# Kernel tuning notes

Measured on AMD Instinct MI355X. Metric: run time of the kernel, lower is better.

The kernel has to match this reference:

```python
import jax, jax.numpy as jnp
import numpy as np

N_LAYERS, HEADS, D_IN, D_OUT, T, D, DFF = 4, 8, 16, 3, 1024, 512, 2048
D_HEAD = D // HEADS


def sinusoidal_pos_enc(t, d):
    # Faithful to the source: base = pos / 10000**(emb_idx/d); sin on even cols, cos on odd cols
    pos = jnp.arange(t, dtype=jnp.float32)[:, None]
    emb = jnp.arange(d, dtype=jnp.float32)[None, :]
    base = pos / jnp.power(10000.0, emb / d)
    even = (jnp.arange(d) % 2 == 0)[None, :]
    return jnp.where(even, jnp.sin(base), jnp.cos(base))  # (t, d)


def layer_norm(x, g, b, eps=1e-5):
    m = x.mean(-1, keepdims=True)
    v = ((x - m) ** 2).mean(-1, keepdims=True)
    return (x - m) / jnp.sqrt(v + eps) * g + b


def setup_inputs() -> dict:
    key = jax.random.key(0)
    ks = iter(jax.random.split(key, 24))
    s = 0.02
    inp = {}
    inp['x'] = jax.random.normal(next(ks), (16, T, D_IN), dtype=jnp.float32)
    inp['pad_mask'] = jax.random.randint(next(ks), (16, T), 0, 2, dtype=jnp.int32)
    inp['enc_W'] = jax.random.normal(next(ks), (D_IN, D), dtype=jnp.float32) * s
    inp['enc_b'] = jnp.zeros((D,), jnp.float32)
    for name in ['Wq', 'Wk', 'Wv', 'Wo']:
        inp[name] = jax.random.normal(next(ks), (N_LAYERS, D, D), dtype=jnp.float32) * s
    inp['ff_W1'] = jax.random.normal(next(ks), (N_LAYERS, D, DFF), dtype=jnp.float32) * s
    inp['ff_b1'] = jnp.zeros((N_LAYERS, DFF), jnp.float32)
    inp['ff_W2'] = jax.random.normal(next(ks), (N_LAYERS, DFF, D), dtype=jnp.float32) * s
    inp['ff_b2'] = jnp.zeros((N_LAYERS, D), jnp.float32)
    inp['ln1_g'] = jnp.ones((N_LAYERS, D), jnp.float32)
    inp['ln1_b'] = jnp.zeros((N_LAYERS, D), jnp.float32)
    inp['ln2_g'] = jnp.ones((N_LAYERS, D), jnp.float32)
    inp['ln2_b'] = jnp.zeros((N_LAYERS, D), jnp.float32)
    inp['out_W'] = jax.random.normal(next(ks), (D * T, D_OUT), dtype=jnp.float32) * s
    inp['out_b'] = jnp.zeros((D_OUT,), jnp.float32)
    return inp


def reference(x, enc_W, enc_b, Wq, Wk, Wv, Wo, ff_W1, ff_b1, ff_W2, ff_b2,
              ln1_g, ln1_b, ln2_g, ln2_b, out_W, out_b, pad_mask):
    n, t = x.shape[0], x.shape[1]
    # InputEncoding (linear) scaled by sqrt(d_model)
    h = (x @ enc_W + enc_b) * jnp.sqrt(jnp.float32(D))
    # Sinusoidal positional encoding, zeroed at masked (pad_mask==0) timesteps
    pe = sinusoidal_pos_enc(t, D)[None]  # (1, t, d)
    pe = jnp.where(pad_mask[..., None] == 0, 0.0, pe)  # (n, t, d)
    h = h + pe
    mask4 = (pad_mask[..., None, None] == 0)  # (n, t, 1, 1)
    for i in range(N_LAYERS):
        # --- MultiHeadAttention (faithful to source's transpose quirk) ---
        Qh = (h @ Wq[i]).reshape(n, t, HEADS, D_HEAD).swapaxes(2, 3)  # (n,t,dh,H)
        Kh = (h @ Wk[i]).reshape(n, t, HEADS, D_HEAD)                 # (n,t,H,dh)
        Vh = (h @ Wv[i]).reshape(n, t, HEADS, D_HEAD).swapaxes(2, 3)  # (n,t,dh,H)
        # energy: per-timestep (dh x dh), scaled by d_head**1/2 == d_head/2 (source precedence)
        energy = jnp.matmul(Qh, Kh) / (D_HEAD / 2.0)                  # (n,t,dh,dh)
        energy = jnp.where(mask4, -1e20, energy)
        attn = jax.nn.softmax(energy, axis=-1)
        head = jnp.matmul(attn, Vh)                                   # (n,t,dh,H)
        out = head.reshape(n, t, D) @ Wo[i]
        # residual + layer norm
        h = layer_norm(out + h, ln1_g[i], ln1_b[i])
        # --- FFN (relu) ---
        ff = jax.nn.relu(h @ ff_W1[i] + ff_b1[i]) @ ff_W2[i] + ff_b2[i]
        h = layer_norm(ff + h, ln2_g[i], ln2_b[i])
    # mode='train': flatten and project
    return h.reshape(n, -1) @ out_W + out_b  # (n, d_output)
```

## Files before the change

kernel.cpp:

```cpp
#include <hip/hip_runtime.h>
#include <cmath>

#define NB 16
#define TSEQ 1024
#define DIN 16
#define DM 512
#define DFFN 2048
#define NLAYERS 4
#define DOUTN 3
#define ROWS (NB*TSEQ)

typedef unsigned short u16;
typedef unsigned int   u32;
typedef short bf16x8 __attribute__((ext_vector_type(8)));
typedef u16   u16x4  __attribute__((ext_vector_type(4)));
typedef float f32x4  __attribute__((ext_vector_type(4)));

__device__ __forceinline__ float b2f(u16 v) { return __uint_as_float((unsigned)v << 16); }
__device__ __forceinline__ u16 f2b(float f) {
    unsigned u = __float_as_uint(f);
    return (u16)((u + 0x7FFFu + ((u >> 16) & 1u)) >> 16);
}

#define GLL(gp, lp) __builtin_amdgcn_global_load_lds( \
    (const __attribute__((address_space(1))) unsigned int*)(gp), \
    (__attribute__((address_space(3))) unsigned int*)(lp), 16, 0, 0)

template<int PERM>
__global__ __launch_bounds__(256) void transpose_cast(
    const float* __restrict__ in, u16* __restrict__ out,
    int K, int N, size_t in_lstride, size_t out_lstride)
{
    in  += (size_t)blockIdx.z * in_lstride;
    out += (size_t)blockIdx.z * out_lstride;
    __shared__ float t[32][33];
    int bk = blockIdx.x * 32, bn = blockIdx.y * 32;
    int x = threadIdx.x & 31, y = threadIdx.x >> 5;
    #pragma unroll
    for (int i = 0; i < 32; i += 8)
        t[y + i][x] = in[(size_t)(bk + y + i) * N + bn + x];
    __syncthreads();
    #pragma unroll
    for (int i = 0; i < 32; i += 8) {
        int row = bn + y + i;
        if (PERM) row = ((row & 63) << 3) | ((row >> 6) & 7);
        out[(size_t)row * K + bk + x] = f2b(t[x][y + i]);
    }
}

__global__ __launch_bounds__(128) void encode_kernel(
    const float* __restrict__ x, const int* __restrict__ pad,
    const float* __restrict__ W, const float* __restrict__ b,
    u16* __restrict__ h)
{
    int row = blockIdx.x;
    int t   = row & (TSEQ - 1);
    int c   = threadIdx.x * 4;
    float acc[4];
    #pragma unroll
    for (int j = 0; j < 4; ++j) acc[j] = b[c + j];
    const float* xr = x + (size_t)row * DIN;
    #pragma unroll
    for (int k = 0; k < DIN; ++k) {
        float xv = xr[k];
        const float* wr = W + (size_t)k * DM + c;
        #pragma unroll
        for (int j = 0; j < 4; ++j) acc[j] += xv * wr[j];
    }
    const float s = 22.62741699796952f;
    bool has_pe = (pad[row] != 0);
    u16x4 o;
    #pragma unroll
    for (int j = 0; j < 4; ++j) {
        acc[j] *= s;
        if (has_pe) {
            int d = c + j;
            float base = (float)t * powf(10000.0f, -(float)d * (1.0f/512.0f));
            acc[j] += ((d & 1) == 0) ? sinf(base) : cosf(base);
        }
        o[j] = f2b(acc[j]);
    }
    *(u16x4*)&h[(size_t)row * DM + c] = o;
}

template<int BIAS, int RELU>
__global__ __launch_bounds__(512, 4) void gemm_bf16(
    const u16* __restrict__ A, const u16* __restrict__ Bt,
    const float* __restrict__ bias, u16* __restrict__ C,
    int M, int N, int K)
{
    __shared__ u16 S[4][8192];
    const int tid  = threadIdx.x;
    const int lane = tid & 63;
    const int wid  = tid >> 6;
    const int wr   = wid >> 2;
    const int wc   = wid & 3;

    const int NY  = N >> 7;
    const int nwg = gridDim.x;
    const int cpx = nwg >> 3;
    const int bid = blockIdx.x;
    const int swz = (bid & 7) * cpx + (bid >> 3);
    const int bm  = (swz / NY) * 128;
    const int bn  = (swz % NY) * 128;

    const int srow8 = lane >> 3;
    const int sslot = lane & 7;
    const int scol  = ((sslot ^ srow8) * 8);
    const u16* Ag = A  + (size_t)(bm + wid * 16 + srow8) * K + scol;
    const u16* Bg = Bt + (size_t)(bn + wid * 16 + srow8) * K + scol;

    f32x4 acc[4][2];
    #pragma unroll
    for (int m = 0; m < 4; ++m)
        #pragma unroll
        for (int n = 0; n < 2; ++n)
            acc[m][n] = (f32x4){0.f, 0.f, 0.f, 0.f};

    const int fr  = lane & 15;
    const int grp = lane >> 4;

    auto STAGE = [&](int k0, int d) {
        u16* Al = S[d * 2 + 0] + wid * 1024;
        u16* Bl = S[d * 2 + 1] + wid * 1024;
        #pragma unroll
        for (int i = 0; i < 2; ++i) {
            GLL(Ag + (size_t)(i * 8) * K + k0, Al + i * 512);
            GLL(Bg + (size_t)(i * 8) * K + k0, Bl + i * 512);
        }
    };

    STAGE(0, 0);
    __syncthreads();

    int cur = 0;
    for (int k0 = 0; k0 < K; k0 += 64) {
        if (k0 + 64 < K) STAGE(k0 + 64, cur ^ 1);
        const u16* As = S[cur * 2 + 0];
        const u16* Bs = S[cur * 2 + 1];
        bf16x8 a[4][2];
        #pragma unroll
        for (int m = 0; m < 4; ++m) {
            int row = wr * 64 + m * 16 + fr;
            #pragma unroll
            for (int ks = 0; ks < 2; ++ks) {
                int slot = (ks * 4 + grp) ^ (row & 7);
                a[m][ks] = *(const bf16x8*)(As + row * 64 + slot * 8);
            }
        }
        #pragma unroll
        for (int n = 0; n < 2; ++n) {
            bf16x8 b[2];
            int row = wc * 32 + n * 16 + fr;
            #pragma unroll
            for (int ks = 0; ks < 2; ++ks) {
                int slot = (ks * 4 + grp) ^ (row & 7);
                b[ks] = *(const bf16x8*)(Bs + row * 64 + slot * 8);
            }
            #pragma unroll
            for (int m = 0; m < 4; ++m) {
                acc[m][n] = __builtin_amdgcn_mfma_f32_16x16x32_bf16(a[m][0], b[0], acc[m][n], 0, 0, 0);
                acc[m][n] = __builtin_amdgcn_mfma_f32_16x16x32_bf16(a[m][1], b[1], acc[m][n], 0, 0, 0);
            }
        }
        __syncthreads();
        cur ^= 1;
    }

    float bb[2] = {0.f, 0.f};
    if (BIAS) {
        #pragma unroll
        for (int n = 0; n < 2; ++n) bb[n] = bias[bn + wc * 32 + n * 16 + fr];
    }
    #pragma unroll
    for (int m = 0; m < 4; ++m) {
        #pragma unroll
        for (int n = 0; n < 2; ++n) {
            int col = bn + wc * 32 + n * 16 + fr;
            #pragma unroll
            for (int j = 0; j < 4; ++j) {
                int row = bm + wr * 64 + m * 16 + grp * 4 + j;
                float v = acc[m][n][j];
                if (BIAS) v += bb[n];
                if (RELU) v = fmaxf(v, 0.f);
                C[(size_t)row * N + col] = f2b(v);
            }
        }
    }
}

__global__ __launch_bounds__(256) void attn_mfma(
    const u16* __restrict__ QKV, const int* __restrict__ pad,
    u16* __restrict__ O)
{
    constexpr int WLDS = 2560;
    __shared__ u16 sh[4 * WLDS];
    const int wid  = threadIdx.x >> 6;
    const int lane = threadIdx.x & 63;
    const int site = blockIdx.x * 4 + wid;
    u16* P2 = sh + wid * WLDS;
    u16* Ol = P2 + 2048;

    const u16* base = QKV + (size_t)site * 1536;
    const int fr  = lane & 15;
    const int grp = lane >> 4;
    const bf16x8 zb = {0,0,0,0,0,0,0,0};
    const f32x4  zf = {0.f,0.f,0.f,0.f};

    if (pad[site] == 0) {
        bf16x8 vv = *(const bf16x8*)(base + 1024 + lane * 8);
        float s = 0.f;
        #pragma unroll
        for (int j = 0; j < 8; ++j) s += b2f((u16)vv[j]);
        s += __shfl_xor(s, 1); s += __shfl_xor(s, 2); s += __shfl_xor(s, 4);
        s *= (1.0f / 64.0f);
        bf16x8 ov;
        #pragma unroll
        for (int h2 = 0; h2 < 8; ++h2) ov[h2] = (short)f2b(__shfl(s, h2 * 8));
        *(bf16x8*)(O + (size_t)site * DM + lane * 8) = ov;
        return;
    }

    bf16x8 kt[4];
    #pragma unroll
    for (int n = 0; n < 4; ++n)
        kt[n] = (grp == 0) ? *(const bf16x8*)(base + 512 + (n * 16 + fr) * 8) : zb;
    bf16x8 bv[2];
    #pragma unroll
    for (int ks = 0; ks < 2; ++ks)
        bv[ks] = (fr < 8) ? *(const bf16x8*)(base + 1024 + fr * 64 + ks * 32 + grp * 8) : zb;

    const int swz = (fr & 3) ^ (fr >> 2);
    u16x4 pk23[4][2];

    #pragma unroll
    for (int m = 0; m < 4; ++m) {
        bf16x8 aq = (grp == 0) ? *(const bf16x8*)(base + (m * 16 + fr) * 8) : zb;
        f32x4 ev[4];
        #pragma unroll
        for (int n = 0; n < 4; ++n)
            ev[n] = __builtin_amdgcn_mfma_f32_16x16x32_bf16(kt[n], aq, zf, 0, 0, 0);
        f32x4 t0, t1;
        #pragma unroll
        for (int j = 0; j < 4; ++j) { t0[j] = fmaxf(ev[0][j], ev[1][j]); t1[j] = fmaxf(ev[2][j], ev[3][j]); }
        float mx = -1e30f;
        #pragma unroll
        for (int j = 0; j < 4; ++j) mx = fmaxf(mx, fmaxf(t0[j], t1[j]));
        mx = fmaxf(mx, __shfl_xor(mx, 16));
        mx = fmaxf(mx, __shfl_xor(mx, 32));
        float p[4][4];
        float s = 0.f;
        #pragma unroll
        for (int n = 0; n < 4; ++n)
            #pragma unroll
            for (int j = 0; j < 4; ++j) {
                p[n][j] = __expf((ev[n][j] - mx) * 0.03125f);
                s += p[n][j];
            }
        s += __shfl_xor(s, 16);
        s += __shfl_xor(s, 32);
        float inv = 1.0f / s;
        u16x4 pk[4];
        #pragma unroll
        for (int n = 0; n < 4; ++n)
            #pragma unroll
            for (int j = 0; j < 4; ++j) pk[n][j] = f2b(p[n][j] * inv);
        int row = m * 16 + fr;
        #pragma unroll
        for (int n = 0; n < 2; ++n) {
            int chunk = (n * 2 + (grp >> 1)) ^ swz;
            *(u16x4*)(P2 + row * 32 + chunk * 8 + (grp & 1) * 4) = pk[n];
        }
        pk23[m][0] = pk[2];
        pk23[m][1] = pk[3];
    }

    f32x4 pv[4];
    #pragma unroll
    for (int m = 0; m < 4; ++m) {
        int row = m * 16 + fr;
        bf16x8 ap = *(const bf16x8*)(P2 + row * 32 + ((grp ^ swz) * 8));
        pv[m] = __builtin_amdgcn_mfma_f32_16x16x32_bf16(ap, bv[0], zf, 0, 0, 0);
    }
    asm volatile("s_waitcnt lgkmcnt(0)" ::: "memory");
    __builtin_amdgcn_sched_barrier(0);

    #pragma unroll
    for (int m = 0; m < 4; ++m) {
        int row = m * 16 + fr;
        #pragma unroll
        for (int n = 0; n < 2; ++n) {
            int chunk = (n * 2 + (grp >> 1)) ^ swz;
            *(u16x4*)(P2 + row * 32 + chunk * 8 + (grp & 1) * 4) = pk23[m][n];
        }
    }
    #pragma unroll
    for (int m = 0; m < 4; ++m) {
        int row = m * 16 + fr;
        bf16x8 ap = *(const bf16x8*)(P2 + row * 32 + ((grp ^ swz) * 8));
        pv[m] = __builtin_amdgcn_mfma_f32_16x16x32_bf16(ap, bv[1], pv[m], 0, 0, 0);
    }

    #pragma unroll
    for (int m = 0; m < 4; ++m)
        #pragma unroll
        for (int j = 0; j < 4; ++j) {
            int row = m * 16 + grp * 4 + j;
            if (fr < 8) Ol[row * 8 + fr] = f2b(pv[m][j]);
        }
    __syncthreads();
    bf16x8 o = *(const bf16x8*)(Ol + lane * 8);
    *(bf16x8*)(O + (size_t)site * DM + lane * 8) = o;
}

__global__ __launch_bounds__(256) void add_ln_kernel(
    const u16* __restrict__ A, u16* __restrict__ H,
    const float* __restrict__ g, const float* __restrict__ b)
{
    int row  = blockIdx.x * 4 + (threadIdx.x >> 6);
    int lane = threadIdx.x & 63;
    const u16* a = A + (size_t)row * DM + lane * 8;
    u16* h = H + (size_t)row * DM + lane * 8;
    bf16x8 av = *(const bf16x8*)a;
    bf16x8 hv = *(const bf16x8*)h;
    float v[8];
    float s = 0.f;
    #pragma unroll
    for (int j = 0; j < 8; ++j) { v[j] = b2f((u16)av[j]) + b2f((u16)hv[j]); s += v[j]; }
    #pragma unroll
    for (int off = 32; off > 0; off >>= 1) s += __shfl_xor(s, off, 64);
    float mean = s * (1.0f / 512.0f);
    float var = 0.f;
    #pragma unroll
    for (int j = 0; j < 8; ++j) { float d = v[j] - mean; var += d * d; }
    #pragma unroll
    for (int off = 32; off > 0; off >>= 1) var += __shfl_xor(var, off, 64);
    float rstd = rsqrtf(var * (1.0f / 512.0f) + 1e-5f);
    bf16x8 ov;
    #pragma unroll
    for (int j = 0; j < 8; ++j) {
        int d = lane * 8 + j;
        ov[j] = (short)f2b((v[j] - mean) * rstd * g[d] + b[d]);
    }
    *(bf16x8*)h = ov;
}

__global__ __launch_bounds__(256) void out_stage1(
    const u16* __restrict__ h, const float* __restrict__ W,
    float* __restrict__ partial)
{
    int b = blockIdx.x, s = blockIdx.y;
    int tid = threadIdx.x;
    const u16* hb = h + (size_t)b * (TSEQ * DM) + (size_t)s * 8192;
    const float* Wb = W + (size_t)s * 8192 * 3;
    float a0 = 0.f, a1 = 0.f, a2 = 0.f;
    #pragma unroll 4
    for (int it = 0; it < 32; ++it) {
        int i = it * 256 + tid;
        float hv = b2f(hb[i]);
        a0 += hv * Wb[i * 3 + 0];
        a1 += hv * Wb[i * 3 + 1];
        a2 += hv * Wb[i * 3 + 2];
    }
    __shared__ float red[3][256];
    red[0][tid] = a0; red[1][tid] = a1; red[2][tid] = a2;
    __syncthreads();
    for (int off = 128; off > 0; off >>= 1) {
        if (tid < off) {
            red[0][tid] += red[0][tid + off];
            red[1][tid] += red[1][tid + off];
            red[2][tid] += red[2][tid + off];
        }
        __syncthreads();
    }
    if (tid == 0) {
        partial[(b * 64 + s) * 3 + 0] = red[0][0];
        partial[(b * 64 + s) * 3 + 1] = red[1][0];
        partial[(b * 64 + s) * 3 + 2] = red[2][0];
    }
}

__global__ __launch_bounds__(64) void out_stage2(
    const float* __restrict__ partial, const float* __restrict__ ob,
    float* __restrict__ out)
{
    int t = threadIdx.x;
    if (t < NB * DOUTN) {
        int b = t / 3, o = t % 3;
        float s = ob[o];
        for (int k = 0; k < 64; ++k) s += partial[(b * 64 + k) * 3 + o];
        out[t] = s;
    }
}

extern "C" void kernel_launch(void* const* d_in, const int* in_sizes, int n_in,
                              void* d_out, int out_size, void* d_ws, size_t ws_size,
                              hipStream_t stream)
{
    const float* x    = (const float*)d_in[0];
    const int*   pad  = (const int*)  d_in[1];
    const float* encW = (const float*)d_in[2];
    const float* encB = (const float*)d_in[3];
    const float* Wq   = (const float*)d_in[4];
    const float* Wk   = (const float*)d_in[5];
    const float* Wv   = (const float*)d_in[6];
    const float* Wo   = (const float*)d_in[7];
    const float* fW1  = (const float*)d_in[8];
    const float* fb1  = (const float*)d_in[9];
    const float* fW2  = (const float*)d_in[10];
    const float* fb2  = (const float*)d_in[11];
    const float* l1g  = (const float*)d_in[12];
    const float* l1b  = (const float*)d_in[13];
    const float* l2g  = (const float*)d_in[14];
    const float* l2b  = (const float*)d_in[15];
    const float* outW = (const float*)d_in[16];
    const float* outB = (const float*)d_in[17];
    float* out = (float*)d_out;

    const size_t WL  = 3145728;
    const size_t BUF = (size_t)ROWS * DM;
    const size_t need = (4 * WL + 6 * BUF) * sizeof(u16);
    if (ws_size < need) return;
    u16* wt = (u16*)d_ws;
    u16* h  = wt + 4 * WL;
    u16* b0 = h  + BUF;
    u16* b3 = b0 + 3 * BUF;
    u16* b4 = b3 + BUF;

    transpose_cast<1><<<dim3(16,16,4), 256, 0, stream>>>(Wq,  wt + 0,       512,  512,  (size_t)512*512,  WL);
    transpose_cast<1><<<dim3(16,16,4), 256, 0, stream>>>(Wk,  wt + 262144,  512,  512,  (size_t)512*512,  WL);
    transpose_cast<0><<<dim3(16,16,4), 256, 0, stream>>>(Wv,  wt + 524288,  512,  512,  (size_t)512*512,  WL);
    transpose_cast<0><<<dim3(16,16,4), 256, 0, stream>>>(Wo,  wt + 786432,  512,  512,  (size_t)512*512,  WL);
    transpose_cast<0><<<dim3(16,64,4), 256, 0, stream>>>(fW1, wt + 1048576, 512,  2048, (size_t)512*2048, WL);
    transpose_cast<0><<<dim3(64,16,4), 256, 0, stream>>>(fW2, wt + 2097152, 2048, 512,  (size_t)2048*512, WL);

    encode_kernel<<<ROWS, 128, 0, stream>>>(x, pad, encW, encB, h);

    for (int l = 0; l < NLAYERS; ++l) {
        u16* wl = wt + (size_t)l * WL;
        gemm_bf16<0,0><<<dim3((ROWS/128)*(1536/128)), 512, 0, stream>>>(h, wl, nullptr, b0, ROWS, 1536, DM);
        attn_mfma<<<ROWS/4, 256, 0, stream>>>(b0, pad, b3);
        gemm_bf16<0,0><<<dim3((ROWS/128)*(DM/128)), 512, 0, stream>>>(b3, wl + 786432, nullptr, b4, ROWS, DM, DM);
        add_ln_kernel<<<ROWS/4, 256, 0, stream>>>(b4, h, l1g + l*DM, l1b + l*DM);
        gemm_bf16<1,1><<<dim3((ROWS/128)*(DFFN/128)), 512, 0, stream>>>(h, wl + 1048576, fb1 + (size_t)l*DFFN, b0, ROWS, DFFN, DM);
        gemm_bf16<1,0><<<dim3((ROWS/128)*(DM/128)), 512, 0, stream>>>(b0, wl + 2097152, fb2 + (size_t)l*DM, b4, ROWS, DM, DFFN);
        add_ln_kernel<<<ROWS/4, 256, 0, stream>>>(b4, h, l2g + l*DM, l2b + l*DM);
    }

    out_stage1<<<dim3(NB, 64), 256, 0, stream>>>(h, outW, (float*)b0);
    out_stage2<<<1, 64, 0, stream>>>((float*)b0, outB, out);
}
```

Baseline: 738.6 us.

## Add triple-buffered BK=32 GEMM with vmcnt-based waits for FFN matmuls

Adds a new GEMM kernel that stages 128x32 tiles of A and B into three LDS buffers with global_load_lds. It uses s_waitcnt vmcnt plus a single barrier per k-step, so loads for step t+2 overlap compute on step t. The smaller LDS footprint allows a launch bound of 6 waves per SIMD. The two FFN GEMMs use the new kernel, while the QKV and output projections keep the original 128x64 double-buffered kernel. The risk is more barriers per unit of K, and correctness of the tail handling depends on nt being of the form 3k+1 (K=512 gives 16, K=2048 gives 64, both fit).

```diff
diff --git a/kernel.cpp b/kernel.cpp
--- a/kernel.cpp
+++ b/kernel.cpp
@@ -26,6 +26,11 @@
     (const __attribute__((address_space(1))) unsigned int*)(gp), \
     (__attribute__((address_space(3))) unsigned int*)(lp), 16, 0, 0)
 
+#define WAITVM2() asm volatile("s_waitcnt vmcnt(2)" ::: "memory")
+#define WAITVM0() asm volatile("s_waitcnt vmcnt(0)" ::: "memory")
+#define BARR() do { asm volatile("" ::: "memory"); __builtin_amdgcn_s_barrier(); \
+                    asm volatile("" ::: "memory"); } while (0)
+
 template<int PERM>
 __global__ __launch_bounds__(256) void transpose_cast(
     const float* __restrict__ in, u16* __restrict__ out,
@@ -84,7 +89,7 @@
 }
 
 template<int BIAS, int RELU>
-__global__ __launch_bounds__(512, 4) void gemm_bf16(
+__global__ __launch_bounds__(512, 4) void gemm128(
     const u16* __restrict__ A, const u16* __restrict__ Bt,
     const float* __restrict__ bias, u16* __restrict__ C,
     int M, int N, int K)
@@ -166,6 +171,109 @@
         __syncthreads();
         cur ^= 1;
     }
+
+    float bb[2] = {0.f, 0.f};
+    if (BIAS) {
+        #pragma unroll
+        for (int n = 0; n < 2; ++n) bb[n] = bias[bn + wc * 32 + n * 16 + fr];
+    }
+    #pragma unroll
+    for (int m = 0; m < 4; ++m) {
+        #pragma unroll
+        for (int n = 0; n < 2; ++n) {
+            int col = bn + wc * 32 + n * 16 + fr;
+            #pragma unroll
+            for (int j = 0; j < 4; ++j) {
+                int row = bm + wr * 64 + m * 16 + grp * 4 + j;
+                float v = acc[m][n][j];
+                if (BIAS) v += bb[n];
+                if (RELU) v = fmaxf(v, 0.f);
+                C[(size_t)row * N + col] = f2b(v);
+            }
+        }
+    }
+}
+
+template<int BIAS, int RELU>
+__global__ __launch_bounds__(512, 6) void gemm3d(
+    const u16* __restrict__ A, const u16* __restrict__ Bt,
+    const float* __restrict__ bias, u16* __restrict__ C,
+    int M, int N, int K)
+{
+    __shared__ u16 S0a[4096], S0b[4096];
+    __shared__ u16 S1a[4096], S1b[4096];
+    __shared__ u16 S2a[4096], S2b[4096];
+    const int tid  = threadIdx.x;
+    const int lane = tid & 63;
+    const int wid  = tid >> 6;
+    const int wr   = wid >> 2;
+    const int wc   = wid & 3;
+
+    const int NY  = N >> 7;
+    const int nwg = gridDim.x;
+    const int cpx = nwg >> 3;
+    const int bid = blockIdx.x;
+    const int swz = (bid & 7) * cpx + (bid >> 3);
+    const int bm  = (swz / NY) * 128;
+    const int bn  = (swz % NY) * 128;
+
+    const int srow   = tid >> 2;
+    const int schunk = (tid & 3) ^ ((srow >> 1) & 3);
+    const u16* Ag = A  + (size_t)(bm + srow) * K + schunk * 8;
+    const u16* Bg = Bt + (size_t)(bn + srow) * K + schunk * 8;
+
+    f32x4 acc[4][2];
+    #pragma unroll
+    for (int m = 0; m < 4; ++m)
+        #pragma unroll
+        for (int n = 0; n < 2; ++n)
+            acc[m][n] = (f32x4){0.f, 0.f, 0.f, 0.f};
+
+    const int fr  = lane & 15;
+    const int grp = lane >> 4;
+
+    const int nt = K >> 5;
+
+#define STAGE3(kt, DA, DB) do { \
+        GLL(Ag + (size_t)(kt) * 32, DA + tid * 8); \
+        GLL(Bg + (size_t)(kt) * 32, DB + tid * 8); } while (0)
+
+#define STEP3(t, RA, RB, SA_, SB_, doStage, last) do { \
+        if (last) { WAITVM0(); } else { WAITVM2(); } \
+        BARR(); \
+        if (doStage) STAGE3((t) + 2, SA_, SB_); \
+        bf16x8 a_[4], b_[2]; \
+        _Pragma("unroll") \
+        for (int m = 0; m < 4; ++m) { \
+            int row = wr * 64 + m * 16 + fr; \
+            int slot = grp ^ ((row >> 1) & 3); \
+            a_[m] = *(const bf16x8*)(RA + row * 32 + slot * 8); \
+        } \
+        _Pragma("unroll") \
+        for (int n = 0; n < 2; ++n) { \
+            int row = wc * 32 + n * 16 + fr; \
+            int slot = grp ^ ((row >> 1) & 3); \
+            b_[n] = *(const bf16x8*)(RB + row * 32 + slot * 8); \
+        } \
+        _Pragma("unroll") \
+        for (int n = 0; n < 2; ++n) \
+            _Pragma("unroll") \
+            for (int m = 0; m < 4; ++m) \
+                acc[m][n] = __builtin_amdgcn_mfma_f32_16x16x32_bf16(a_[m], b_[n], acc[m][n], 0, 0, 0); \
+    } while (0)
+
+    STAGE3(0, S0a, S0b);
+    STAGE3(1, S1a, S1b);
+
+    for (int it = 0; it + 3 < nt; it += 3) {
+        STEP3(it + 0, S0a, S0b, S2a, S2b, (it + 2 < nt), false);
+        STEP3(it + 1, S1a, S1b, S0a, S0b, (it + 3 < nt), false);
+        STEP3(it + 2, S2a, S2b, S1a, S1b, (it + 4 < nt), false);
+    }
+    STEP3(nt - 1, S0a, S0b, S1a, S1b, false, true);
+
+#undef STEP3
+#undef STAGE3
 
     float bb[2] = {0.f, 0.f};
     if (BIAS) {
@@ -438,12 +546,12 @@
 
     for (int l = 0; l < NLAYERS; ++l) {
         u16* wl = wt + (size_t)l * WL;
-        gemm_bf16<0,0><<<dim3((ROWS/128)*(1536/128)), 512, 0, stream>>>(h, wl, nullptr, b0, ROWS, 1536, DM);
+        gemm128<0,0><<<dim3((ROWS/128)*(1536/128)), 512, 0, stream>>>(h, wl, nullptr, b0, ROWS, 1536, DM);
         attn_mfma<<<ROWS/4, 256, 0, stream>>>(b0, pad, b3);
-        gemm_bf16<0,0><<<dim3((ROWS/128)*(DM/128)), 512, 0, stream>>>(b3, wl + 786432, nullptr, b4, ROWS, DM, DM);
+        gemm128<0,0><<<dim3((ROWS/128)*(DM/128)), 512, 0, stream>>>(b3, wl + 786432, nullptr, b4, ROWS, DM, DM);
         add_ln_kernel<<<ROWS/4, 256, 0, stream>>>(b4, h, l1g + l*DM, l1b + l*DM);
-        gemm_bf16<1,1><<<dim3((ROWS/128)*(DFFN/128)), 512, 0, stream>>>(h, wl + 1048576, fb1 + (size_t)l*DFFN, b0, ROWS, DFFN, DM);
-        gemm_bf16<1,0><<<dim3((ROWS/128)*(DM/128)), 512, 0, stream>>>(b0, wl + 2097152, fb2 + (size_t)l*DM, b4, ROWS, DM, DFFN);
+        gemm3d<1,1><<<dim3((ROWS/128)*(DFFN/128)), 512, 0, stream>>>(h, wl + 1048576, fb1 + (size_t)l*DFFN, b0, ROWS, DFFN, DM);
+        gemm3d<1,0><<<dim3((ROWS/128)*(DM/128)), 512, 0, stream>>>(b0, wl + 2097152, fb2 + (size_t)l*DM, b4, ROWS, DM, DFFN);
         add_ln_kernel<<<ROWS/4, 256, 0, stream>>>(b4, h, l2g + l*DM, l2b + l*DM);
     }
 
```

Result: slower. 915.9 us (+24.0%).
